# Kernel tuning notes

Measured on AMD Instinct MI355X. Metric: run time of the kernel, lower is better.

The kernel has to match this reference:

```python
import jax, jax.numpy as jnp
import numpy as np

B = 48            # graph pairs
NQ, NC = 20, 16   # query / corpus node counts (corpus padded to NMAX)
NMAX = 20         # max_node_set_size
DN, DE = 16, 8    # raw node / edge feature dims
D = 32            # node_state_dim
EH = 64           # edge_hidden_sizes[-1]
EQ, EC = 80, 60   # edges per query / corpus graph
PROP = 5          # n_prop_layers
TEMP = 0.01       # sinkhorn temperature
ITERS = 20        # sinkhorn iterations
LAMBDA = 1.0
NTOT = B * (NQ + NC)
NE = B * (EQ + EC)
SRC, DST = np.triu_indices(NMAX, 1)   # nC2 = 190 node pairs
_indq = np.ones(NMAX, np.int32)
_indc = np.array([1] * NC + [0] * (NMAX - NC), np.int32)
NXOR = jnp.asarray((_indq[:, None] ^ _indc[None, :]).astype(np.float32))  # [20,20]


def _mlp2(x, w1, b1, w2, b2):
    return jnp.maximum(x @ w1 + b1, 0.0) @ w2 + b2


def _sinkhorn(log_alpha):
    la = log_alpha / TEMP
    for _ in range(ITERS):
        la = la - jax.nn.logsumexp(la, axis=2, keepdims=True)
        la = la - jax.nn.logsumexp(la, axis=1, keepdims=True)
    return jnp.exp(la)


def _edge_emb(H, adj, w1, b1, w2, b2):
    s, d = H[:, SRC], H[:, DST]            # [B,nC2,D] gathers
    e = adj[:, SRC, DST][..., None]        # [B,nC2,1]
    f = _mlp2(jnp.concatenate([s, d, e], -1), w1, b1, w2, b2)
    bk = _mlp2(jnp.concatenate([d, s, e], -1), w1, b1, w2, b2)
    return f + bk                          # bidirectional msg, [B,nC2,EH]


def _forward(node_features, edge_features, query_adj, corpus_adj,
             enc_nw, enc_nb, enc_ew, enc_eb,
             msg_w1, msg_b1, msg_w2, msg_b2,
             upd_w1, upd_b1, upd_w2, upd_b2,
             sink_w1, sink_b1, sink_w2, sink_b2,
             lrl_w1, lrl_b1, lrl_w2, lrl_b2,
             from_idx, to_idx):
    h = node_features @ enc_nw + enc_nb    # GMN encoder (linear MLPs)
    e = edge_features @ enc_ew + enc_eb
    for _ in range(PROP):                  # shared-param propagation
        msg = _mlp2(jnp.concatenate([h[from_idx], h[to_idx], e], -1),
                    msg_w1, msg_b1, msg_w2, msg_b2)
        agg = jax.ops.segment_sum(msg, to_idx, num_segments=NTOT)
        h = h + _mlp2(jnp.concatenate([agg, h], -1), upd_w1, upd_b1, upd_w2, upd_b2)
    hp = h.reshape(B, NQ + NC, D)          # split_and_stack (static sizes)
    Hq = hp[:, :NQ]
    Hc = jnp.pad(hp[:, NQ:], ((0, 0), (0, NMAX - NC), (0, 0)))
    tq = _mlp2(Hq, sink_w1, sink_b1, sink_w2, sink_b2)
    tc = _mlp2(Hc, sink_w1, sink_b1, sink_w2, sink_b2)
    cost = jnp.abs(tq[:, :, None, :] - tc[:, None, :, :]).sum(-1)  # cdist p=1
    P = _sinkhorn(-cost)                   # node transport plan [B,20,20]
    Eq = _edge_emb(Hq, query_adj, lrl_w1, lrl_b1, lrl_w2, lrl_b2)
    Ec = _edge_emb(Hc, corpus_adj, lrl_w1, lrl_b1, lrl_w2, lrl_b2)
    Pa, Pb = P[:, SRC, :], P[:, DST, :]
    straight = Pa[:, :, SRC] * Pb[:, :, DST]    # plan[src_i,src_j]*plan[dst_i,dst_j]
    cross = Pa[:, :, DST] * Pb[:, :, SRC]
    eT = straight + cross                  # use_max=False, no second sinkhorn
    aq = query_adj[:, SRC, DST].astype(jnp.int32)
    ac = corpus_adj[:, SRC, DST].astype(jnp.int32)
    pxor = (aq[:, :, None] ^ ac[:, None, :]).astype(P.dtype)
    ediff = Eq[:, :, None, :] - Ec[:, None, :, :]   # [B,nC2,nC2,EH]
    ecost = jnp.maximum(ediff, 0.0).sum(-1) + jnp.maximum(-ediff, 0.0).sum(-1)
    edge_align = (pxor * eT * ecost).sum((-1, -2))
    ndiff = Hq[:, :, None, :] - Hc[:, None, :, :]   # [B,20,20,D]
    ncost = jnp.maximum(ndiff, 0.0).sum(-1) + jnp.maximum(-ndiff, 0.0).sum(-1)
    node_align = (NXOR * P * ncost).sum((-1, -2))
    return edge_align + LAMBDA * node_align         # [B]


def setup_inputs():
    key = jax.random.key(0)
    rng = np.random.default_rng(0)
    base = (np.arange(B) * (NQ + NC))[:, None]
    fq = base + rng.integers(0, NQ, (B, EQ)); tq = base + rng.integers(0, NQ, (B, EQ))
    fc = base + NQ + rng.integers(0, NC, (B, EC)); tc = base + NQ + rng.integers(0, NC, (B, EC))
    from_idx = jnp.asarray(np.concatenate([fq, fc], 1).reshape(-1), jnp.int32)
    to_idx = jnp.asarray(np.concatenate([tq, tc], 1).reshape(-1), jnp.int32)
    qadj = rng.integers(0, 2, (B, NMAX, NMAX)).astype(np.float32)
    cadj = rng.integers(0, 2, (B, NMAX, NMAX)).astype(np.float32)
    cadj[:, NC:, :] = 0.0; cadj[:, :, NC:] = 0.0   # padded corpus nodes have no edges
    ks = iter(jax.random.split(key, 32))
    def w(shape, s=0.1):
        return jax.random.normal(next(ks), shape, jnp.float32) * s
    return {
        'node_features': w((NTOT, DN), 1.0),
        'edge_features': w((NE, DE), 1.0),
        'query_adj': jnp.asarray(qadj),
        'corpus_adj': jnp.asarray(cadj),
        'enc_nw': w((DN, D)), 'enc_nb': w((D,)),
        'enc_ew': w((DE, 16)), 'enc_eb': w((16,)),
        'msg_w1': w((2 * D + 16, EH)), 'msg_b1': w((EH,)),
        'msg_w2': w((EH, EH)), 'msg_b2': w((EH,)),
        'upd_w1': w((EH + D, EH)), 'upd_b1': w((EH,)),
        'upd_w2': w((EH, D)), 'upd_b2': w((D,)),
        'sink_w1': w((D, NMAX)), 'sink_b1': w((NMAX,)),
        'sink_w2': w((NMAX, NMAX)), 'sink_b2': w((NMAX,)),
        'lrl_w1': w((2 * D + 1, EH)), 'lrl_b1': w((EH,)),
        'lrl_w2': w((EH, EH)), 'lrl_b2': w((EH,)),
        'from_idx': from_idx, 'to_idx': to_idx,
        'graph_sizes': jnp.asarray(np.tile([NQ, NC], B), jnp.int32),
    }


def reference(node_features, edge_features, query_adj, corpus_adj,
              enc_nw, enc_nb, enc_ew, enc_eb,
              msg_w1, msg_b1, msg_w2, msg_b2,
              upd_w1, upd_b1, upd_w2, upd_b2,
              sink_w1, sink_b1, sink_w2, sink_b2,
              lrl_w1, lrl_b1, lrl_w2, lrl_b2,
              from_idx, to_idx, graph_sizes):
    return _forward(node_features, edge_features, query_adj, corpus_adj,
                    enc_nw, enc_nb, enc_ew, enc_eb,
                    msg_w1, msg_b1, msg_w2, msg_b2,
                    upd_w1, upd_b1, upd_w2, upd_b2,
                    sink_w1, sink_b1, sink_w2, sink_b2,
                    lrl_w1, lrl_b1, lrl_w2, lrl_b2,
                    from_idx, to_idx)
```

## Files before the change

### kernel.cpp

```cpp
#include <hip/hip_runtime.h>


constexpr int kB    = 48;
constexpr int kNM   = 20;
constexpr int kD    = 32;
constexpr int kNP   = 190;
constexpr int kNTOT = 1728;
constexpr int kIters = 20;
constexpr float kInvT = 100.0f;

__device__ __forceinline__ void pair_sd(int p, int& s, int& d) {
    int row = 0, rem = p;
    #pragma unroll
    for (int r = 0; r < 19; ++r) {
        int len = 19 - r;
        if (rem < len) { row = r; break; }
        rem -= len;
    }
    s = row; d = row + 1 + rem;
}

__device__ __forceinline__ float bc(float v, int k) {
    return __int_as_float(__builtin_amdgcn_readlane(__float_as_int(v), k));
}

__device__ __forceinline__ void lse20(float (&r)[20]) {
    float m01 = fmaxf(r[0], r[1]),  m23 = fmaxf(r[2], r[3]),
          m45 = fmaxf(r[4], r[5]),  m67 = fmaxf(r[6], r[7]),
          m89 = fmaxf(r[8], r[9]),  mab = fmaxf(r[10], r[11]),
          mcd = fmaxf(r[12], r[13]), mef = fmaxf(r[14], r[15]),
          mgh = fmaxf(r[16], r[17]), mij = fmaxf(r[18], r[19]);
    float n0 = fmaxf(m01, m23), n1 = fmaxf(m45, m67), n2 = fmaxf(m89, mab),
          n3 = fmaxf(mcd, mef), n4 = fmaxf(mgh, mij);
    float m = fmaxf(fmaxf(fmaxf(n0, n1), fmaxf(n2, n3)), n4);
    float e[20];
    #pragma unroll
    for (int k = 0; k < 20; ++k) e[k] = __expf(r[k] - m);
    float s01 = e[0] + e[1],  s23 = e[2] + e[3],  s45 = e[4] + e[5],
          s67 = e[6] + e[7],  s89 = e[8] + e[9],  sab = e[10] + e[11],
          scd = e[12] + e[13], sef = e[14] + e[15], sgh = e[16] + e[17],
          sij = e[18] + e[19];
    float t0 = s01 + s23, t1 = s45 + s67, t2 = s89 + sab,
          t3 = scd + sef, t4 = sgh + sij;
    float s = ((t0 + t1) + (t2 + t3)) + t4;
    float l = m + __logf(s);
    #pragma unroll
    for (int k = 0; k < 20; ++k) r[k] -= l;
}

__global__ void k_enc(const float* __restrict__ nf, const float* __restrict__ nw,
                      const float* __restrict__ nb, const float* __restrict__ ef,
                      const float* __restrict__ ew, const float* __restrict__ eb,
                      float* __restrict__ h, float* __restrict__ ee,
                      float* __restrict__ agg, float* __restrict__ out) {
    int tid = blockIdx.x * 256 + threadIdx.x;
    int stride = gridDim.x * 256;
    for (int i = tid; i < kNTOT * 32; i += stride) {
        int n = i >> 5, c = i & 31;
        float acc = nb[c];
        const float* row = nf + n * 16;
        #pragma unroll
        for (int k = 0; k < 16; ++k) acc = fmaf(row[k], nw[k * 32 + c], acc);
        h[i] = acc;
    }
    for (int i = tid; i < 6720 * 16; i += stride) {
        int n = i >> 4, c = i & 15;
        float acc = eb[c];
        const float* row = ef + n * 8;
        #pragma unroll
        for (int k = 0; k < 8; ++k) acc = fmaf(row[k], ew[k * 16 + c], acc);
        ee[i] = acc;
    }
    for (int i = tid; i < kNTOT * 64; i += stride) agg[i] = 0.f;
    if (tid < kB) out[tid] = 0.f;
}

__global__ void __launch_bounds__(256)
k_msg(const float* __restrict__ h, const float* __restrict__ ee,
      const int* __restrict__ fidx, const int* __restrict__ tidx,
      const float* __restrict__ w1, const float* __restrict__ b1,
      const float* __restrict__ w2, const float* __restrict__ b2,
      float* __restrict__ agg) {
    int w = threadIdx.x >> 6, lane = threadIdx.x & 63;
    int e0 = (blockIdx.x * 4 + w) * 2;
    int toj[2]; float xa[2], xb[2], acc[2], o[2];
    #pragma unroll
    for (int j = 0; j < 2; ++j) {
        int e = e0 + j;
        int fr = fidx[e]; toj[j] = tidx[e];
        xa[j] = h[(lane < 32 ? fr : toj[j]) * kD + (lane & 31)];
        xb[j] = ee[e * 16 + (lane & 15)];
        acc[j] = b1[lane];
    }
    #pragma unroll
    for (int k = 0; k < 64; ++k) {
        float w1k = w1[k * 64 + lane];
        #pragma unroll
        for (int j = 0; j < 2; ++j) acc[j] = fmaf(bc(xa[j], k), w1k, acc[j]);
    }
    #pragma unroll
    for (int k = 0; k < 16; ++k) {
        float w1k = w1[(64 + k) * 64 + lane];
        #pragma unroll
        for (int j = 0; j < 2; ++j) acc[j] = fmaf(bc(xb[j], k), w1k, acc[j]);
    }
    #pragma unroll
    for (int j = 0; j < 2; ++j) { acc[j] = fmaxf(acc[j], 0.f); o[j] = b2[lane]; }
    #pragma unroll
    for (int k = 0; k < 64; ++k) {
        float w2k = w2[k * 64 + lane];
        #pragma unroll
        for (int j = 0; j < 2; ++j) o[j] = fmaf(bc(acc[j], k), w2k, o[j]);
    }
    #pragma unroll
    for (int j = 0; j < 2; ++j) atomicAdd(&agg[toj[j] * 64 + lane], o[j]);
}

__global__ void __launch_bounds__(256)
k_upd(float* __restrict__ h, float* __restrict__ agg,
      const float* __restrict__ w1, const float* __restrict__ b1,
      const float* __restrict__ w2, const float* __restrict__ b2) {
    int w = threadIdx.x >> 6, lane = threadIdx.x & 63;
    int n0 = (blockIdx.x * 4 + w) * 2;
    float xa[2], xb[2], acc[2], o[2];
    #pragma unroll
    for (int j = 0; j < 2; ++j) {
        int n = n0 + j;
        xa[j] = agg[n * 64 + lane];
        agg[n * 64 + lane] = 0.f;
        xb[j] = h[n * kD + (lane & 31)];
        acc[j] = b1[lane];
    }
    #pragma unroll
    for (int k = 0; k < 64; ++k) {
        float w1k = w1[k * 64 + lane];
        #pragma unroll
        for (int j = 0; j < 2; ++j) acc[j] = fmaf(bc(xa[j], k), w1k, acc[j]);
    }
    #pragma unroll
    for (int k = 0; k < 32; ++k) {
        float w1k = w1[(64 + k) * 64 + lane];
        #pragma unroll
        for (int j = 0; j < 2; ++j) acc[j] = fmaf(bc(xb[j], k), w1k, acc[j]);
    }
    #pragma unroll
    for (int j = 0; j < 2; ++j) { acc[j] = fmaxf(acc[j], 0.f); o[j] = b2[lane & 31]; }
    #pragma unroll
    for (int k = 0; k < 64; ++k) {
        float w2k = w2[k * 32 + (lane & 31)];
        #pragma unroll
        for (int j = 0; j < 2; ++j) o[j] = fmaf(bc(acc[j], k), w2k, o[j]);
    }
    if (lane < 32) {
        #pragma unroll
        for (int j = 0; j < 2; ++j) h[(n0 + j) * kD + lane] += o[j];
    }
}

__global__ void __launch_bounds__(256)
k_tail(const float* __restrict__ h,
       const float* __restrict__ w1, const float* __restrict__ b1,
       const float* __restrict__ w2, const float* __restrict__ b2,
       float* __restrict__ Hq, float* __restrict__ Hc,
       float* __restrict__ P, float* __restrict__ out) {
    __shared__ float tqS[400], tcS[400];
    __shared__ float trS[20 * 21];
    int b = blockIdx.x;
    int t = threadIdx.x, lane = t & 63, wave = t >> 6;

    for (int task = wave; task < 40; task += 4) {
        int side = task >= 20, i = task - side * 20;
        float v = 0.f;
        if (lane < 32) {
            if (!side)        v = h[(b * 36 + i) * kD + lane];
            else if (i < 16)  v = h[(b * 36 + 20 + i) * kD + lane];
            (side ? Hc : Hq)[(b * kNM + i) * kD + lane] = v;
        }
        int tt = lane < 20 ? lane : 0;
        float acc = b1[tt];
        #pragma unroll
        for (int k = 0; k < 32; ++k) acc = fmaf(bc(v, k), w1[k * 20 + tt], acc);
        acc = fmaxf(acc, 0.f);
        float o = b2[tt];
        #pragma unroll
        for (int k = 0; k < 20; ++k) o = fmaf(bc(acc, k), w2[k * 20 + tt], o);
        if (lane < 20) (side ? tcS : tqS)[i * 20 + lane] = o;
    }
    __syncthreads();

    float r[20];
    if (t < 20) {
        float tqr[20];
        #pragma unroll
        for (int k = 0; k < 20; ++k) tqr[k] = tqS[t * 20 + k];
        #pragma unroll
        for (int j = 0; j < 20; ++j) {
            float c = 0.f;
            #pragma unroll
            for (int k = 0; k < 20; ++k) c += fabsf(tqr[k] - tcS[j * 20 + k]);
            r[j] = -c * kInvT;
        }
    }
    for (int it = 0; it < kIters; ++it) {
        if (t < 20) {
            lse20(r);
            #pragma unroll
            for (int j = 0; j < 20; ++j) trS[t * 21 + j] = r[j];
        }
        __syncthreads();
        if (t < 20) {
            #pragma unroll
            for (int i = 0; i < 20; ++i) r[i] = trS[i * 21 + t];
            lse20(r);
            #pragma unroll
            for (int i = 0; i < 20; ++i) trS[i * 21 + t] = r[i];
        }
        __syncthreads();
        if (t < 20) {
            #pragma unroll
            for (int j = 0; j < 20; ++j) r[j] = trS[t * 21 + j];
        }
        __syncthreads();
    }
    float part = 0.f;
    if (t < 20) {
        float pv[20];
        #pragma unroll
        for (int j = 0; j < 20; ++j) pv[j] = __expf(r[j]);
        float* Pb = P + b * 400 + t * 20;
        #pragma unroll
        for (int j = 0; j < 20; ++j) Pb[j] = pv[j];
        float pr4 = (pv[16] + pv[17]) + (pv[18] + pv[19]);
        float l1 = 0.f;
        const float* hq = h + (b * 36 + t) * kD;
        #pragma unroll
        for (int k = 0; k < 32; ++k) l1 += fabsf(hq[k]);
        part = pr4 * l1;
    }
    if (t < 64) {
        #pragma unroll
        for (int off = 32; off; off >>= 1) part += __shfl_down(part, off, 64);
        if (t == 0) atomicAdd(&out[b], part);
    }
}

__global__ void __launch_bounds__(256)
k_edge_emb(const float* __restrict__ Hq, const float* __restrict__ Hc,
           const float* __restrict__ qadj, const float* __restrict__ cadj,
           const float* __restrict__ w1, const float* __restrict__ b1,
           const float* __restrict__ w2, const float* __restrict__ b2,
           float* __restrict__ Eq, float* __restrict__ EcT) {
    int w = threadIdx.x >> 6, lane = threadIdx.x & 63;
    int xcd = blockIdx.x & 7, slot = blockIdx.x >> 3;
    int b = xcd + 8 * (slot / 24);
    int r = slot % 24;
    float xa[4], ev[4], af[4], ab[4];
    int sidej[4], pj[4];
    #pragma unroll
    for (int j = 0; j < 4; ++j) {
        int tloc = r * 16 + w * 4 + j;
        if (tloc >= 380) tloc = 379;
        sidej[j] = tloc / kNP; pj[j] = tloc % kNP;
        int s, d; pair_sd(pj[j], s, d);
        const float* H = sidej[j] ? Hc : Hq;
        xa[j] = (lane < 32) ? H[(b * kNM + s) * kD + lane]
                            : H[(b * kNM + d) * kD + (lane - 32)];
        ev[j] = (sidej[j] ? cadj : qadj)[b * 400 + s * 20 + d];
        float bb = b1[lane];
        af[j] = bb; ab[j] = bb;
    }
    #pragma unroll
    for (int k = 0; k < 64; ++k) {
        float w1k = w1[k * 64 + lane];
        #pragma unroll
        for (int j = 0; j < 4; ++j) {
            af[j] = fmaf(bc(xa[j], k),      w1k, af[j]);
            ab[j] = fmaf(bc(xa[j], k ^ 32), w1k, ab[j]);
        }
    }
    {
        float w1e = w1[64 * 64 + lane];
        #pragma unroll
        for (int j = 0; j < 4; ++j) {
            af[j] = fmaf(ev[j], w1e, af[j]);
            ab[j] = fmaf(ev[j], w1e, ab[j]);
        }
    }
    float hid[4], o[4];
    #pragma unroll
    for (int j = 0; j < 4; ++j) {
        hid[j] = fmaxf(af[j], 0.f) + fmaxf(ab[j], 0.f);
        o[j] = 2.f * b2[lane];
    }
    #pragma unroll
    for (int k = 0; k < 64; ++k) {
        float w2k = w2[k * 64 + lane];
        #pragma unroll
        for (int j = 0; j < 4; ++j) o[j] = fmaf(bc(hid[j], k), w2k, o[j]);
    }
    #pragma unroll
    for (int j = 0; j < 4; ++j) {
        if (sidej[j]) EcT[(b * 64 + lane) * kNP + pj[j]] = o[j];
        else          Eq[(b * kNP + pj[j]) * 64 + lane] = o[j];
    }
}

#define EC64(X) X(0) X(1) X(2) X(3) X(4) X(5) X(6) X(7) X(8) X(9) X(10) X(11) \
  X(12) X(13) X(14) X(15) X(16) X(17) X(18) X(19) X(20) X(21) X(22) X(23) \
  X(24) X(25) X(26) X(27) X(28) X(29) X(30) X(31) X(32) X(33) X(34) X(35) \
  X(36) X(37) X(38) X(39) X(40) X(41) X(42) X(43) X(44) X(45) X(46) X(47) \
  X(48) X(49) X(50) X(51) X(52) X(53) X(54) X(55) X(56) X(57) X(58) X(59) \
  X(60) X(61) X(62) X(63)

__global__ void __launch_bounds__(256)
k_final(const float* __restrict__ P, const float* __restrict__ Eq,
        const float* __restrict__ EcT, const float* __restrict__ qadj,
        const float* __restrict__ cadj, float* __restrict__ out) {
    __shared__ float Ps[400];
    __shared__ unsigned char spsh[192], dpsh[192];
    int xcd = blockIdx.x & 7, slot = blockIdx.x >> 3;
    int b = xcd + 8 * (slot / 6);
    int r = slot % 6;
    int qt = r >> 1, ph = r & 1;
    int t = threadIdx.x, w = t >> 6, lane = t & 63;
    if (t < 192) {
        int s = 0, d = 0;
        if (t < kNP) pair_sd(t, s, d);
        spsh[t] = (unsigned char)s;
        dpsh[t] = (unsigned char)d;
    }
    for (int i = t; i < 400; i += 256) Ps[i] = P[b * 400 + i];
    __syncthreads();

    int q = qt * 64 + lane;
    bool qv = q < kNP;
    int qc = qv ? q : 0;
    int sq = spsh[qc], dq = dpsh[qc];
    float acv = qv ? cadj[b * 400 + sq * 20 + dq] : 0.f;

    const float* ecb = EcT + b * 64 * kNP + qc;
#define ECD(i) float ec##i = ecb[(i) * kNP];
    EC64(ECD)
#undef ECD

    float acc = 0.f;
    for (int p = ph * 4 + w; p < kNP; p += 8) {
        int sp = spsh[p], dp = dpsh[p];
        float aq = qadj[b * 400 + sp * 20 + dp];
        const float4* eqr = (const float4*)(Eq + (b * kNP + p) * 64);
        float ce0 = 0.f, ce1 = 0.f;
#define QS(k, i0, i1, i2, i3) { float4 e = eqr[k]; \
        ce0 += fabsf(e.x - ec##i0) + fabsf(e.y - ec##i1); \
        ce1 += fabsf(e.z - ec##i2) + fabsf(e.w - ec##i3); }
        QS(0,0,1,2,3)     QS(1,4,5,6,7)     QS(2,8,9,10,11)    QS(3,12,13,14,15)
        QS(4,16,17,18,19) QS(5,20,21,22,23) QS(6,24,25,26,27)  QS(7,28,29,30,31)
        QS(8,32,33,34,35) QS(9,36,37,38,39) QS(10,40,41,42,43) QS(11,44,45,46,47)
        QS(12,48,49,50,51) QS(13,52,53,54,55) QS(14,56,57,58,59) QS(15,60,61,62,63)
#undef QS
        float eT = Ps[sp * 20 + sq] * Ps[dp * 20 + dq]
                 + Ps[sp * 20 + dq] * Ps[dp * 20 + sq];
        float gate = (aq > 0.5f) ? (1.f - acv) : acv;
        float wq = qv ? gate * eT : 0.f;
        acc = fmaf(wq, ce0 + ce1, acc);
    }
    #pragma unroll
    for (int off = 32; off; off >>= 1) acc += __shfl_down(acc, off, 64);
    if (lane == 0) atomicAdd(&out[b], acc);
}

extern "C" void kernel_launch(void* const* d_in, const int* in_sizes, int n_in,
                              void* d_out, int out_size, void* d_ws, size_t ws_size,
                              hipStream_t stream) {
    auto f = [&](int i) { return (const float*)d_in[i]; };
    const float* nf   = f(0);
    const float* ef   = f(1);
    const float* qadj = f(2);
    const float* cadj = f(3);
    const int* from_idx = (const int*)d_in[24];
    const int* to_idx   = (const int*)d_in[25];
    float* out = (float*)d_out;

    float* ws  = (float*)d_ws;
    float* h   = ws;
    float* ee  = h   + 55296;
    float* agg = ee  + 107520;
    float* Hq  = agg + 110592;
    float* Hc  = Hq  + 30720;
    float* P   = Hc  + 30720;
    float* Eq  = P   + 19200;
    float* EcT = Eq  + 583680;

    k_enc<<<432, 256, 0, stream>>>(nf, f(4), f(5), ef, f(6), f(7), h, ee, agg, out);
    for (int it = 0; it < 5; ++it) {
        k_msg<<<840, 256, 0, stream>>>(h, ee, from_idx, to_idx,
                                       f(8), f(9), f(10), f(11), agg);
        k_upd<<<216, 256, 0, stream>>>(h, agg, f(12), f(13), f(14), f(15));
    }
    k_tail<<<48, 256, 0, stream>>>(h, f(16), f(17), f(18), f(19), Hq, Hc, P, out);
    k_edge_emb<<<1152, 256, 0, stream>>>(Hq, Hc, qadj, cadj,
                                         f(20), f(21), f(22), f(23), Eq, EcT);
    k_final<<<288, 256, 0, stream>>>(P, Eq, EcT, qadj, cadj, out);
}
```

Before: 160.3 us.

## Store corpus edge embeddings row-major and remap final kernel lanes to features

The edge-embedding kernel now writes corpus embeddings in the same [pair, feature] layout as the query embeddings, replacing the transposed, strided EcT stores with coalesced ones. k_final is reorganised so each lane owns one feature dimension and holds 32 corpus-pair values in registers. Per-pair weights are broadcast via readlane into four independent accumulators, and the Eq row and adjacency value for the next query pair are software-prefetched. Launch bounds request 4 blocks per SM. The cost is more readlane traffic and lanes 32–63 doing duplicate weight computation.

```diff
diff --git a/kernel.cpp b/kernel.cpp
--- a/kernel.cpp
+++ b/kernel.cpp
@@ -249,7 +249,7 @@
            const float* __restrict__ qadj, const float* __restrict__ cadj,
            const float* __restrict__ w1, const float* __restrict__ b1,
            const float* __restrict__ w2, const float* __restrict__ b2,
-           float* __restrict__ Eq, float* __restrict__ EcT) {
+           float* __restrict__ Eq, float* __restrict__ Ec) {
     int w = threadIdx.x >> 6, lane = threadIdx.x & 63;
     int xcd = blockIdx.x & 7, slot = blockIdx.x >> 3;
     int b = xcd + 8 * (slot / 24);
@@ -299,29 +299,22 @@
         for (int j = 0; j < 4; ++j) o[j] = fmaf(bc(hid[j], k), w2k, o[j]);
     }
     #pragma unroll
-    for (int j = 0; j < 4; ++j) {
-        if (sidej[j]) EcT[(b * 64 + lane) * kNP + pj[j]] = o[j];
-        else          Eq[(b * kNP + pj[j]) * 64 + lane] = o[j];
-    }
-}
-
-#define EC64(X) X(0) X(1) X(2) X(3) X(4) X(5) X(6) X(7) X(8) X(9) X(10) X(11) \
+    for (int j = 0; j < 4; ++j)
+        (sidej[j] ? Ec : Eq)[(b * kNP + pj[j]) * 64 + lane] = o[j];
+}
+
+#define EC_ALL(X) X(0) X(1) X(2) X(3) X(4) X(5) X(6) X(7) X(8) X(9) X(10) X(11) \
   X(12) X(13) X(14) X(15) X(16) X(17) X(18) X(19) X(20) X(21) X(22) X(23) \
-  X(24) X(25) X(26) X(27) X(28) X(29) X(30) X(31) X(32) X(33) X(34) X(35) \
-  X(36) X(37) X(38) X(39) X(40) X(41) X(42) X(43) X(44) X(45) X(46) X(47) \
-  X(48) X(49) X(50) X(51) X(52) X(53) X(54) X(55) X(56) X(57) X(58) X(59) \
-  X(60) X(61) X(62) X(63)
-
-__global__ void __launch_bounds__(256)
+  X(24) X(25) X(26) X(27) X(28) X(29) X(30) X(31)
+
+__global__ void __launch_bounds__(256, 4)
 k_final(const float* __restrict__ P, const float* __restrict__ Eq,
-        const float* __restrict__ EcT, const float* __restrict__ qadj,
+        const float* __restrict__ Ec, const float* __restrict__ qadj,
         const float* __restrict__ cadj, float* __restrict__ out) {
     __shared__ float Ps[400];
     __shared__ unsigned char spsh[192], dpsh[192];
     int xcd = blockIdx.x & 7, slot = blockIdx.x >> 3;
-    int b = xcd + 8 * (slot / 6);
-    int r = slot % 6;
-    int qt = r >> 1, ph = r & 1;
+    int b = xcd + 8 * (slot / 6), qt = slot % 6;
     int t = threadIdx.x, w = t >> 6, lane = t & 63;
     if (t < 192) {
         int s = 0, d = 0;
@@ -332,40 +325,45 @@
     for (int i = t; i < 400; i += 256) Ps[i] = P[b * 400 + i];
     __syncthreads();
 
-    int q = qt * 64 + lane;
+    int l31 = lane & 31;
+    int q = qt * 32 + l31;
     bool qv = q < kNP;
-    int qc = qv ? q : 0;
-    int sq = spsh[qc], dq = dpsh[qc];
+    int sq = spsh[qv ? q : 0], dq = dpsh[qv ? q : 0];
     float acv = qv ? cadj[b * 400 + sq * 20 + dq] : 0.f;
 
-    const float* ecb = EcT + b * 64 * kNP + qc;
-#define ECD(i) float ec##i = ecb[(i) * kNP];
-    EC64(ECD)
-#undef ECD
-
-    float acc = 0.f;
-    for (int p = ph * 4 + w; p < kNP; p += 8) {
-        int sp = spsh[p], dp = dpsh[p];
-        float aq = qadj[b * 400 + sp * 20 + dp];
-        const float4* eqr = (const float4*)(Eq + (b * kNP + p) * 64);
-        float ce0 = 0.f, ce1 = 0.f;
-#define QS(k, i0, i1, i2, i3) { float4 e = eqr[k]; \
-        ce0 += fabsf(e.x - ec##i0) + fabsf(e.y - ec##i1); \
-        ce1 += fabsf(e.z - ec##i2) + fabsf(e.w - ec##i3); }
-        QS(0,0,1,2,3)     QS(1,4,5,6,7)     QS(2,8,9,10,11)    QS(3,12,13,14,15)
-        QS(4,16,17,18,19) QS(5,20,21,22,23) QS(6,24,25,26,27)  QS(7,28,29,30,31)
-        QS(8,32,33,34,35) QS(9,36,37,38,39) QS(10,40,41,42,43) QS(11,44,45,46,47)
-        QS(12,48,49,50,51) QS(13,52,53,54,55) QS(14,56,57,58,59) QS(15,60,61,62,63)
-#undef QS
+    const float* ecb = Ec + (b * kNP + qt * 32) * 64 + lane;
+#define EC_DECL(i) float ec##i = (qt * 32 + i < kNP) ? ecb[i * 64] : 0.f;
+    EC_ALL(EC_DECL)
+#undef EC_DECL
+
+    float a0 = 0.f, a1 = 0.f, a2 = 0.f, a3 = 0.f;
+    int pp = w;
+    float aqc = qadj[b * 400 + spsh[pp] * 20 + dpsh[pp]];
+    float eqc = Eq[(b * kNP + pp) * 64 + lane];
+    while (pp < kNP) {
+        int pn = pp + 4;
+        float aqn = 0.f, eqn = 0.f;
+        if (pn < kNP) {
+            aqn = qadj[b * 400 + spsh[pn] * 20 + dpsh[pn]];
+            eqn = Eq[(b * kNP + pn) * 64 + lane];
+        }
+        int sp = spsh[pp], dp = dpsh[pp];
         float eT = Ps[sp * 20 + sq] * Ps[dp * 20 + dq]
                  + Ps[sp * 20 + dq] * Ps[dp * 20 + sq];
-        float gate = (aq > 0.5f) ? (1.f - acv) : acv;
-        float wq = qv ? gate * eT : 0.f;
-        acc = fmaf(wq, ce0 + ce1, acc);
-    }
-    #pragma unroll
-    for (int off = 32; off; off >>= 1) acc += __shfl_down(acc, off, 64);
-    if (lane == 0) atomicAdd(&out[b], acc);
+        float wqv = qv ? ((aqc > 0.5f) ? (1.f - acv) : acv) * eT : 0.f;
+#define EC_FMA(i) { float d_ = fabsf(eqc - ec##i); \
+        if ((i & 3) == 0) a0 = fmaf(bc(wqv, i), d_, a0); \
+        else if ((i & 3) == 1) a1 = fmaf(bc(wqv, i), d_, a1); \
+        else if ((i & 3) == 2) a2 = fmaf(bc(wqv, i), d_, a2); \
+        else a3 = fmaf(bc(wqv, i), d_, a3); }
+        EC_ALL(EC_FMA)
+#undef EC_FMA
+        aqc = aqn; eqc = eqn; pp = pn;
+    }
+    float partial = (a0 + a1) + (a2 + a3);
+    #pragma unroll
+    for (int off = 32; off; off >>= 1) partial += __shfl_down(partial, off, 64);
+    if (lane == 0) atomicAdd(&out[b], partial);
 }
 
 extern "C" void kernel_launch(void* const* d_in, const int* in_sizes, int n_in,
@@ -388,7 +386,7 @@
     float* Hc  = Hq  + 30720;
     float* P   = Hc  + 30720;
     float* Eq  = P   + 19200;
-    float* EcT = Eq  + 583680;
+    float* Ec  = Eq  + 583680;
 
     k_enc<<<432, 256, 0, stream>>>(nf, f(4), f(5), ef, f(6), f(7), h, ee, agg, out);
     for (int it = 0; it < 5; ++it) {
@@ -398,6 +396,6 @@
     }
     k_tail<<<48, 256, 0, stream>>>(h, f(16), f(17), f(18), f(19), Hq, Hc, P, out);
     k_edge_emb<<<1152, 256, 0, stream>>>(Hq, Hc, qadj, cadj,
-                                         f(20), f(21), f(22), f(23), Eq, EcT);
-    k_final<<<288, 256, 0, stream>>>(P, Eq, EcT, qadj, cadj, out);
-}
+                                         f(20), f(21), f(22), f(23), Eq, Ec);
+    k_final<<<288, 256, 0, stream>>>(P, Eq, Ec, qadj, cadj, out);
+}
```

After: 159.7 us. Within noise of the previous version (-0.4%).
